# Performance work log

Measured on AMD Instinct MI355X. Metric: run time of the kernel, lower is better.

Reference implementation:

```python
import jax, jax.numpy as jnp
import numpy as np

N, D, H, R = 50000, 256, 4, 3
C = D // H        # head dim = 64
E = 400000        # edges per relation
NEG = 0.2         # LeakyReLU slope
LN_EPS = 1e-5


def _segment_softmax(att, seg, n):
    # att: [E, H], seg: [E] destination node ids -> softmax per (node, head)
    m = jax.ops.segment_max(att, seg, num_segments=n)
    m = jnp.where(jnp.isfinite(m), m, 0.0)        # nodes with no edges
    e = jnp.exp(att - m[seg])
    s = jax.ops.segment_sum(e, seg, num_segments=n)
    return e / (s[seg] + 1e-16)


def setup_inputs() -> dict:
    key = jax.random.key(0)
    ks = jax.random.split(key, 16)
    inp = {
        'feat': jax.random.normal(ks[0], (N, D), jnp.float32),
        'Wl': jax.random.normal(ks[1], (D, D), jnp.float32) / np.sqrt(D).astype(np.float32),
        'bl': jnp.zeros((D,), jnp.float32),
        'Wr': jax.random.normal(ks[2], (D, D), jnp.float32) / np.sqrt(D).astype(np.float32),
        'br': jnp.zeros((D,), jnp.float32),
        'attn_l': jax.random.normal(ks[3], (R, H, C), jnp.float32) / np.sqrt(C).astype(np.float32),
        'attn_r': jax.random.normal(ks[4], (R, H, C), jnp.float32) / np.sqrt(C).astype(np.float32),
        'rel_q': jax.random.normal(ks[5], (H, C), jnp.float32) / np.sqrt(C).astype(np.float32),
        'rel_k': jax.random.normal(ks[6], (H, C), jnp.float32) / np.sqrt(C).astype(np.float32),
        'ln_gamma': jnp.ones((D,), jnp.float32),
        'ln_beta': jnp.zeros((D,), jnp.float32),
    }
    for r in range(R):
        inp[f'edge_src_{r}'] = jax.random.randint(ks[7 + 2 * r], (E,), 0, N, jnp.int64 if jax.config.jax_enable_x64 else jnp.int32)
        inp[f'edge_dst_{r}'] = jax.random.randint(ks[8 + 2 * r], (E,), 0, N, jnp.int64 if jax.config.jax_enable_x64 else jnp.int32)
    return inp


def reference(feat, Wl, bl, Wr, br, attn_l, attn_r, rel_q, rel_k, ln_gamma, ln_beta,
              edge_src_0, edge_dst_0, edge_src_1, edge_dst_1, edge_src_2, edge_dst_2):
    # per-node-type linear projections -> multi-head [N, H, C]
    k = (feat @ Wl + bl).reshape(N, H, C)
    v = (feat @ Wr + br).reshape(N, H, C)
    srcs = [edge_src_0, edge_src_1, edge_src_2]
    dsts = [edge_dst_0, edge_dst_1, edge_dst_2]
    rel_outs = []
    for r in range(R):  # loop over fixed, structurally distinct relations
        s, d = srcs[r], dsts[r]
        # edge attention: (k_src . a_l) + (v_dst . a_r), LeakyReLU (attn_dropout inactive in eval)
        att = jnp.einsum('ehc,hc->eh', k[s], attn_l[r]) + jnp.einsum('ehc,hc->eh', v[d], attn_r[r])
        att = jax.nn.leaky_relu(att, NEG)
        a = _segment_softmax(att, d, N)                                   # [E, H]
        # message 'h' is edges.dst['v'] in the original code (faithful)
        h = jax.ops.segment_sum(a[:, :, None] * v[d], d, num_segments=N)  # [N, H, C]
        rel_outs.append(h)
    # stack relation embeddings + self 'v' (the +1 none-selection relation)
    x = jnp.stack(rel_outs + [v], axis=1)                                  # [N, T=R+1, H, C]
    # MetapathGATConv (1 layer) stand-in: self embedding queries all relations per head
    q = jnp.einsum('nhc,hc->nh', x[:, -1], rel_q)                          # [N, H]
    kk = jnp.einsum('nthc,hc->nth', x, rel_k)                              # [N, T, H]
    beta = jax.nn.softmax(jax.nn.leaky_relu(q[:, None, :] + kk, NEG), axis=1)  # [N, T, H]
    out = jnp.einsum('nth,nthc->nhc', beta, x).reshape(N, D)
    # activation -> (dropout inactive in eval) -> LayerNorm
    out = jax.nn.relu(out)
    mu = out.mean(-1, keepdims=True)
    var = out.var(-1, keepdims=True)
    out = (out - mu) * jax.lax.rsqrt(var + LN_EPS) * ln_gamma + ln_beta
    return out
```

## Files before the change

kernel.cpp:

```cpp
#include <hip/hip_runtime.h>

#define N_NODES 50000
#define DIM 256
#define NEG 0.2f
#define LN_EPS 1e-5f
#define SCAT_BLOCKS 2048

typedef __attribute__((ext_vector_type(8))) short short8;
typedef __attribute__((ext_vector_type(4))) float f32x4;

__device__ __forceinline__ unsigned short f2bf(float x) {
    unsigned int u = __builtin_bit_cast(unsigned int, x);
    u += 0x7fffu + ((u >> 16) & 1u);
    return (unsigned short)(u >> 16);
}

__device__ __forceinline__ void load_lds16(const void* g, void* l) {
    __builtin_amdgcn_global_load_lds((const unsigned int*)g, (unsigned int*)l, 16, 0, 0);
}

__device__ __forceinline__ short8 cvt_bfrag(float4 a4, float4 b4) {
    short8 r;
    r[0] = (short)f2bf(a4.x); r[1] = (short)f2bf(a4.y);
    r[2] = (short)f2bf(a4.z); r[3] = (short)f2bf(a4.w);
    r[4] = (short)f2bf(b4.x); r[5] = (short)f2bf(b4.y);
    r[6] = (short)f2bf(b4.z); r[7] = (short)f2bf(b4.w);
    return r;
}

__global__ __launch_bounds__(256) void prep(
    const float* __restrict__ Wr, unsigned short* __restrict__ WrF,
    const int* __restrict__ d0, const int* __restrict__ d1, const int* __restrict__ d2,
    int E, unsigned char* __restrict__ mask)
{
    if (blockIdx.x < 32) {
        const int o    = blockIdx.x * 256 + threadIdx.x;
        const int lane = o & 63;
        const int frag = o >> 6;
        const int mt = frag & 15, kk = frag >> 4;
        const int ln = lane & 15, quad = lane >> 4;
        const float* src = Wr + (size_t)(kk * 32 + quad * 8) * DIM + mt * 16 + ln;
        short8 v;
        #pragma unroll
        for (int j = 0; j < 8; ++j) v[j] = (short)f2bf(src[(size_t)j * DIM]);
        *(short8*)(WrF + (size_t)o * 8) = v;
    } else {
        const int total = 3 * E;
        for (int i = (blockIdx.x - 32) * 256 + (int)threadIdx.x; i < total;
             i += SCAT_BLOCKS * 256) {
            const int* d; int base, e;
            if (i >= 2 * E)  { d = d2; e = i - 2 * E; base = 2 * N_NODES; }
            else if (i >= E) { d = d1; e = i - E;     base = N_NODES; }
            else             { d = d0; e = i;         base = 0; }
            mask[base + d[e]] = (unsigned char)1;
        }
    }
}

__global__ __launch_bounds__(256, 2) void fused_mfma(
    const float* __restrict__ feat, const unsigned short* __restrict__ WrF,
    const float* __restrict__ br, const float* __restrict__ rel_q,
    const float* __restrict__ rel_k, const float* __restrict__ gamma,
    const float* __restrict__ beta_p, const unsigned char* __restrict__ mask,
    float* __restrict__ out)
{
    __shared__ unsigned short lds[40960];
    const int lane = threadIdx.x & 63;
    const int wave = threadIdx.x >> 6;
    const int ln = lane & 15;
    const int quad = lane >> 4;
    int node = blockIdx.x * 64 + wave * 16 + ln;
    const bool valid = node < N_NODES;
    if (!valid) node = N_NODES - 1;

    {
        const char* g = (const char*)WrF;
        #pragma unroll
        for (int r = 0; r < 16; ++r) {
            const int off = wave * 16384 + r * 1024;
            load_lds16(g + off + lane * 16, (char*)lds + off);
        }
        #pragma unroll
        for (int r = 0; r < 4; ++r) {
            const int off = wave * 4096 + r * 1024;
            load_lds16(g + 65536 + off + lane * 16, (char*)lds + 65536 + off);
        }
    }

    const int m0 = (int)mask[node];
    const int m1 = (int)mask[N_NODES + node];
    const int m2 = (int)mask[2 * N_NODES + node];

    const float* fptr = feat + (size_t)node * DIM + quad * 8;
    float4 F0[8], F1[8];
    #pragma unroll
    for (int kk = 0; kk < 8; ++kk) {
        F0[kk] = *(const float4*)(fptr + kk * 32);
        F1[kk] = *(const float4*)(fptr + kk * 32 + 4);
    }
    short8 bfr[8];
    #pragma unroll
    for (int kk = 0; kk < 8; ++kk) bfr[kk] = cvt_bfrag(F0[kk], F1[kk]);

    f32x4 acc[16];
    #pragma unroll
    for (int mt = 0; mt < 16; ++mt) acc[mt] = (f32x4){0.f, 0.f, 0.f, 0.f};

    __syncthreads();

    #pragma unroll
    for (int kk = 0; kk < 4; ++kk) {
        #pragma unroll
        for (int mt = 0; mt < 16; ++mt) {
            const short8 a = *(const short8*)((const char*)lds
                               + (kk * 16 + mt) * 1024 + lane * 16);
            acc[mt] = __builtin_amdgcn_mfma_f32_16x16x32_bf16(a, bfr[kk], acc[mt], 0, 0, 0);
        }
    }

    __syncthreads();

    {
        const char* g = (const char*)WrF + 81920;
        #pragma unroll
        for (int r = 0; r < 12; ++r) {
            const int off = (wave * 12 + r) * 1024;
            load_lds16(g + off + lane * 16, (char*)lds + off);
        }
    }
    #pragma unroll
    for (int mt = 0; mt < 16; ++mt) {
        const short8 a = *(const short8*)((const char*)lds
                           + 65536 + mt * 1024 + lane * 16);
        acc[mt] = __builtin_amdgcn_mfma_f32_16x16x32_bf16(a, bfr[4], acc[mt], 0, 0, 0);
    }

    __syncthreads();

    #pragma unroll
    for (int kk = 5; kk < 8; ++kk) {
        #pragma unroll
        for (int mt = 0; mt < 16; ++mt) {
            const short8 a = *(const short8*)((const char*)lds
                               + ((kk - 5) * 16 + mt) * 1024 + lane * 16);
            acc[mt] = __builtin_amdgcn_mfma_f32_16x16x32_bf16(a, bfr[kk], acc[mt], 0, 0, 0);
        }
    }

    float qp[4] = {0.f, 0.f, 0.f, 0.f}, kp[4] = {0.f, 0.f, 0.f, 0.f};
    #pragma unroll
    for (int mt = 0; mt < 16; ++mt) {
        const int cbase = mt * 16 + quad * 4;
        const float4 bb = *(const float4*)(br + cbase);
        acc[mt][0] += bb.x; acc[mt][1] += bb.y; acc[mt][2] += bb.z; acc[mt][3] += bb.w;
        const float4 rq = *(const float4*)(rel_q + cbase);
        const float4 rk = *(const float4*)(rel_k + cbase);
        const int h = mt >> 2;
        qp[h] += acc[mt][0] * rq.x + acc[mt][1] * rq.y + acc[mt][2] * rq.z + acc[mt][3] * rq.w;
        kp[h] += acc[mt][0] * rk.x + acc[mt][1] * rk.y + acc[mt][2] * rk.z + acc[mt][3] * rk.w;
    }
    #pragma unroll
    for (int h = 0; h < 4; ++h) {
        qp[h] += __shfl_xor(qp[h], 16); qp[h] += __shfl_xor(qp[h], 32);
        kp[h] += __shfl_xor(kp[h], 16); kp[h] += __shfl_xor(kp[h], 32);
    }

    const int cnt = m0 + m1 + m2;

    float wgt[4];
    #pragma unroll
    for (int h = 0; h < 4; ++h) {
        const float q = qp[h];
        const float qk = q + kp[h];
        const float a = q  > 0.f ? q  : NEG * q;
        const float b = qk > 0.f ? qk : NEG * qk;
        const float mx = fmaxf(a, b);
        const float eb = (float)(cnt + 1) * __expf(b - mx);
        const float ea = (float)(3 - cnt) * __expf(a - mx);
        wgt[h] = eb / (eb + ea);
    }

    float sum = 0.f, ssq = 0.f;
    #pragma unroll
    for (int mt = 0; mt < 16; ++mt) {
        const float w = wgt[mt >> 2];
        #pragma unroll
        for (int r = 0; r < 4; ++r) {
            float v = fmaxf(acc[mt][r] * w, 0.f);
            acc[mt][r] = v;
            sum += v; ssq += v * v;
        }
    }
    sum += __shfl_xor(sum, 16); sum += __shfl_xor(sum, 32);
    ssq += __shfl_xor(ssq, 16); ssq += __shfl_xor(ssq, 32);
    const float mu = sum * (1.f / 256.f);
    const float var = ssq * (1.f / 256.f) - mu * mu;
    const float rstd = rsqrtf(var + LN_EPS);

    #pragma unroll
    for (int mt = 0; mt < 16; ++mt) {
        const int cbase = mt * 16 + quad * 4;
        const float4 g = *(const float4*)(gamma + cbase);
        const float4 b = *(const float4*)(beta_p + cbase);
        acc[mt][0] = (acc[mt][0] - mu) * rstd * g.x + b.x;
        acc[mt][1] = (acc[mt][1] - mu) * rstd * g.y + b.y;
        acc[mt][2] = (acc[mt][2] - mu) * rstd * g.z + b.z;
        acc[mt][3] = (acc[mt][3] - mu) * rstd * g.w + b.w;
    }

    __syncthreads();
    {
        char* slice = (char*)lds + wave * 16384;
        #pragma unroll
        for (int mt = 0; mt < 16; ++mt) {
            const int col = (mt * 64 + quad * 16) ^ ((ln & 7) << 4);
            *(f32x4*)(slice + ln * 1024 + col) = acc[mt];
        }
        asm volatile("s_waitcnt lgkmcnt(0)" ::: "memory");
        __builtin_amdgcn_sched_barrier(0);
        const int base_node = blockIdx.x * 64 + wave * 16;
        #pragma unroll
        for (int r = 0; r < 16; ++r) {
            if (base_node + r < N_NODES) {
                const int off = (lane * 16) ^ ((r & 7) << 4);
                const float4 v = *(const float4*)(slice + r * 1024 + off);
                *(float4*)(out + (size_t)(base_node + r) * DIM + lane * 4) = v;
            }
        }
    }
}

extern "C" void kernel_launch(void* const* d_in, const int* in_sizes, int n_in,
                              void* d_out, int out_size, void* d_ws, size_t ws_size,
                              hipStream_t stream) {
    const float* feat  = (const float*)d_in[0];
    const float* Wr    = (const float*)d_in[3];
    const float* br    = (const float*)d_in[4];
    const float* rel_q = (const float*)d_in[7];
    const float* rel_k = (const float*)d_in[8];
    const float* gamma = (const float*)d_in[9];
    const float* beta  = (const float*)d_in[10];
    const int* dst0 = (const int*)d_in[12];
    const int* dst1 = (const int*)d_in[14];
    const int* dst2 = (const int*)d_in[16];
    const int E = in_sizes[12];

    unsigned short* WrF = (unsigned short*)d_ws;
    unsigned char* mask = (unsigned char*)d_ws + DIM * DIM * 2;

    hipMemsetAsync(mask, 0, 150016, stream);
    prep<<<32 + SCAT_BLOCKS, 256, 0, stream>>>(Wr, WrF, dst0, dst1, dst2, E, mask);
    fused_mfma<<<(N_NODES + 63) / 64, 256, 0, stream>>>(
        feat, WrF, br, rel_q, rel_k, gamma, beta, mask, (float*)d_out);
}
```

Before: 156.1 us.

## Double-buffer weight K-slices in LDS and stage feature fragments in shared memory

Replaces the three-phase weight staging (80KB then 48KB reload) with a 32KB double buffer that streams one 16KB K-slice per iteration while the current slice feeds MFMAs. The bf16 feature fragments move from registers into LDS and are read back each iteration. LDS drops from 80KB to 64KB, aiming to lower register pressure and overlap weight loads with compute. In exchange it adds a barrier per K-step and a rolled loop, which may cost issue overhead and latency exposure.

Result: no change. 156.3 us (+0.1%).

```diff
diff --git a/kernel.cpp b/kernel.cpp
--- a/kernel.cpp
+++ b/kernel.cpp
@@ -64,7 +64,8 @@
     const float* __restrict__ beta_p, const unsigned char* __restrict__ mask,
     float* __restrict__ out)
 {
-    __shared__ unsigned short lds[40960];
+    __shared__ unsigned short lds[32768];
+    char* const base = (char*)lds;
     const int lane = threadIdx.x & 63;
     const int wave = threadIdx.x >> 6;
     const int ln = lane & 15;
@@ -76,14 +77,9 @@
     {
         const char* g = (const char*)WrF;
         #pragma unroll
-        for (int r = 0; r < 16; ++r) {
-            const int off = wave * 16384 + r * 1024;
-            load_lds16(g + off + lane * 16, (char*)lds + off);
-        }
-        #pragma unroll
         for (int r = 0; r < 4; ++r) {
             const int off = wave * 4096 + r * 1024;
-            load_lds16(g + 65536 + off + lane * 16, (char*)lds + 65536 + off);
+            load_lds16(g + off + lane * 16, base + 32768 + off);
         }
     }
 
@@ -92,59 +88,45 @@
     const int m2 = (int)mask[2 * N_NODES + node];
 
     const float* fptr = feat + (size_t)node * DIM + quad * 8;
-    float4 F0[8], F1[8];
-    #pragma unroll
+    char* const fw = base + wave * 8192 + lane * 16;
+    #pragma unroll
+    for (int c = 0; c < 2; ++c) {
+        float4 F0[4], F1[4];
+        #pragma unroll
+        for (int k = 0; k < 4; ++k) {
+            F0[k] = *(const float4*)(fptr + (c * 4 + k) * 32);
+            F1[k] = *(const float4*)(fptr + (c * 4 + k) * 32 + 4);
+        }
+        #pragma unroll
+        for (int k = 0; k < 4; ++k)
+            *(short8*)(fw + (c * 4 + k) * 1024) = cvt_bfrag(F0[k], F1[k]);
+    }
+
+    f32x4 acc[16];
+    #pragma unroll
+    for (int mt = 0; mt < 16; ++mt) acc[mt] = (f32x4){0.f, 0.f, 0.f, 0.f};
+
+    __syncthreads();
+
+    #pragma unroll 1
     for (int kk = 0; kk < 8; ++kk) {
-        F0[kk] = *(const float4*)(fptr + kk * 32);
-        F1[kk] = *(const float4*)(fptr + kk * 32 + 4);
-    }
-    short8 bfr[8];
-    #pragma unroll
-    for (int kk = 0; kk < 8; ++kk) bfr[kk] = cvt_bfrag(F0[kk], F1[kk]);
-
-    f32x4 acc[16];
-    #pragma unroll
-    for (int mt = 0; mt < 16; ++mt) acc[mt] = (f32x4){0.f, 0.f, 0.f, 0.f};
-
-    __syncthreads();
-
-    #pragma unroll
-    for (int kk = 0; kk < 4; ++kk) {
+        if (kk < 7) {
+            const char* g = (const char*)WrF + (kk + 1) * 16384;
+            char* l = base + 32768 + (((kk + 1) & 1) << 14);
+            #pragma unroll
+            for (int r = 0; r < 4; ++r) {
+                const int off = wave * 4096 + r * 1024;
+                load_lds16(g + off + lane * 16, l + off);
+            }
+        }
+        const short8 bq = *(const short8*)(base + wave * 8192 + kk * 1024 + lane * 16);
+        const char* wb = base + 32768 + ((kk & 1) << 14) + lane * 16;
         #pragma unroll
         for (int mt = 0; mt < 16; ++mt) {
-            const short8 a = *(const short8*)((const char*)lds
-                               + (kk * 16 + mt) * 1024 + lane * 16);
-            acc[mt] = __builtin_amdgcn_mfma_f32_16x16x32_bf16(a, bfr[kk], acc[mt], 0, 0, 0);
-        }
-    }
-
-    __syncthreads();
-
-    {
-        const char* g = (const char*)WrF + 81920;
-        #pragma unroll
-        for (int r = 0; r < 12; ++r) {
-            const int off = (wave * 12 + r) * 1024;
-            load_lds16(g + off + lane * 16, (char*)lds + off);
-        }
-    }
-    #pragma unroll
-    for (int mt = 0; mt < 16; ++mt) {
-        const short8 a = *(const short8*)((const char*)lds
-                           + 65536 + mt * 1024 + lane * 16);
-        acc[mt] = __builtin_amdgcn_mfma_f32_16x16x32_bf16(a, bfr[4], acc[mt], 0, 0, 0);
-    }
-
-    __syncthreads();
-
-    #pragma unroll
-    for (int kk = 5; kk < 8; ++kk) {
-        #pragma unroll
-        for (int mt = 0; mt < 16; ++mt) {
-            const short8 a = *(const short8*)((const char*)lds
-                               + ((kk - 5) * 16 + mt) * 1024 + lane * 16);
-            acc[mt] = __builtin_amdgcn_mfma_f32_16x16x32_bf16(a, bfr[kk], acc[mt], 0, 0, 0);
-        }
+            const short8 a = *(const short8*)(wb + mt * 1024);
+            acc[mt] = __builtin_amdgcn_mfma_f32_16x16x32_bf16(a, bq, acc[mt], 0, 0, 0);
+        }
+        __syncthreads();
     }
 
     float qp[4] = {0.f, 0.f, 0.f, 0.f}, kp[4] = {0.f, 0.f, 0.f, 0.f};
@@ -210,7 +192,7 @@
 
     __syncthreads();
     {
-        char* slice = (char*)lds + wave * 16384;
+        char* slice = base + wave * 16384;
         #pragma unroll
         for (int mt = 0; mt < 16; ++mt) {
             const int col = (mt * 64 + quad * 16) ^ ((ln & 7) << 4);
```
